# Kernel optimization log

Measured on AMD Instinct MI355X. Metric: run time of the kernel, lower is better.

The kernel has to match this reference:

```python
import jax, jax.numpy as jnp
import numpy as np

D = 128  # head dim

def setup_inputs() -> dict:
    key = jax.random.key(0)
    k1, k2, k3, k4, k5 = jax.random.split(key, 5)
    B, N, M, C1, C2 = 4, 4096, 4096, 1024, 1024
    x = jax.random.normal(k1, (B, N, C1), dtype=jnp.float32)
    y = jax.random.normal(k2, (B, M, C2), dtype=jnp.float32)
    # Linear(c, d, bias=False): out = inp @ W where W is [c, d]
    Wq = jax.random.normal(k3, (C1, D), dtype=jnp.float32) / np.sqrt(C1)
    Wk = jax.random.normal(k4, (C2, D), dtype=jnp.float32) / np.sqrt(C2)
    Wv = jax.random.normal(k5, (C2, D), dtype=jnp.float32) / np.sqrt(C2)
    return {"x": x, "y": y, "Wq": Wq, "Wk": Wk, "Wv": Wv}

def reference(x, y, Wq, Wk, Wv):
    q = x @ Wq                               # [B, N, d]
    k = y @ Wk                               # [B, M, d]
    v = y @ Wv                               # [B, M, d]
    scale = 1.0 / jnp.sqrt(jnp.asarray(D, dtype=q.dtype))
    a = jnp.einsum('bnd,bmd->bnm', q, k) * scale
    a = jax.nn.softmax(a, axis=-1)           # softmax FIRST
    a = jnp.triu(a, k=1)                     # post-softmax causal mask (keeps strict upper)
    out = jnp.einsum('bnm,bmd->bnd', a, v)   # [B, N, d]
    return out
```

## Files before the change

### kernel.cpp

```cpp
#include <hip/hip_runtime.h>
#include <hip/hip_bf16.h>
#include <stdint.h>


typedef __attribute__((ext_vector_type(8))) __bf16    bf16x8;
typedef __attribute__((ext_vector_type(4))) float     floatx4;
typedef __attribute__((ext_vector_type(8))) uint16_t  u16x8;
typedef __attribute__((ext_vector_type(4))) uint32_t  u32x4;

#define DEVFN __device__ __forceinline__

DEVFN uint16_t f32_to_bf16(float f) {
  uint32_t u = __builtin_bit_cast(uint32_t, f);
  u += 0x7FFFu + ((u >> 16) & 1u);
  return (uint16_t)(u >> 16);
}

DEVFN uint32_t bcast(float f) { return __builtin_bit_cast(uint32_t, f); }

DEVFN u32x4 pack_bf16_8(float4 a0, float4 a1) {
  uint32_t b0 = bcast(a0.x) + 0x8000u, b1 = bcast(a0.y) + 0x8000u;
  uint32_t b2 = bcast(a0.z) + 0x8000u, b3 = bcast(a0.w) + 0x8000u;
  uint32_t b4 = bcast(a1.x) + 0x8000u, b5 = bcast(a1.y) + 0x8000u;
  uint32_t b6 = bcast(a1.z) + 0x8000u, b7 = bcast(a1.w) + 0x8000u;
  u32x4 o;
  o[0] = (b0 >> 16) | (b1 & 0xFFFF0000u);
  o[1] = (b2 >> 16) | (b3 & 0xFFFF0000u);
  o[2] = (b4 >> 16) | (b5 & 0xFFFF0000u);
  o[3] = (b6 >> 16) | (b7 & 0xFFFF0000u);
  return o;
}

__global__ __launch_bounds__(256) void wt_kernel(
    const float* __restrict__ Wq, const float* __restrict__ Wk,
    const float* __restrict__ Wv, uint16_t* __restrict__ wt) {
  int tid = blockIdx.x * 256 + threadIdx.x;
  int mat = tid >> 14;
  int rem = tid & 16383;
  int n  = rem & 127;
  int k0 = rem >> 7;
  const float* W = (mat == 0) ? Wq : ((mat == 1) ? Wk : Wv);
  u16x8 v;
#pragma unroll
  for (int j = 0; j < 8; ++j) v[j] = f32_to_bf16(W[(k0 * 8 + j) * 128 + n]);
  *(u16x8*)&wt[mat * (128 * 1024) + n * 1024 + k0 * 8] = v;
}

__global__ __launch_bounds__(256) void qkv_kernel(
    const float* __restrict__ x, const float* __restrict__ y,
    const uint16_t* __restrict__ wt, uint16_t* __restrict__ q,
    uint16_t* __restrict__ k, uint16_t* __restrict__ vt) {
  constexpr int LDT = 72;
  constexpr int ABUF = 128 * LDT;
  __shared__ __align__(16) uint16_t sA[2 * ABUF];
  __shared__ __align__(16) uint16_t sW[2 * ABUF];
  const int t = threadIdx.x;
  const int mat = blockIdx.y, rt = blockIdx.x;
  const float* A = (mat == 0) ? x : y;
  const uint16_t* Wt = wt + mat * (128 * 1024);
  const int lane = t & 63, wv = t >> 6;
  const int cidx = lane & 15, quad = lane >> 4;
  const int sr = t >> 3;
  const int sc = (t & 7) * 8;
  const int Arow0 = rt * 128;

  floatx4 acc[2][8];
#pragma unroll
  for (int rg = 0; rg < 2; ++rg)
#pragma unroll
    for (int ng = 0; ng < 8; ++ng) acc[rg][ng] = (floatx4){0.f, 0.f, 0.f, 0.f};

  float4 a0r[4], a1r[4];
  u16x8 wr[4];
#pragma unroll
  for (int u = 0; u < 4; ++u) {
    int row = u * 32 + sr;
    const float* ap = &A[(size_t)(Arow0 + row) * 1024 + sc];
    a0r[u] = *(const float4*)ap;
    a1r[u] = *(const float4*)(ap + 4);
    wr[u]  = *(const u16x8*)&Wt[row * 1024 + sc];
  }
#pragma unroll
  for (int u = 0; u < 4; ++u) {
    int row = u * 32 + sr;
    *(u32x4*)&sA[row * LDT + sc] = pack_bf16_8(a0r[u], a1r[u]);
    *(u16x8*)&sW[row * LDT + sc] = wr[u];
  }
  __syncthreads();

  for (int kt = 0; kt < 16; ++kt) {
    const int cur = kt & 1, nxt = cur ^ 1;
    if (kt < 15) {
      const int kc = (kt + 1) * 64;
#pragma unroll
      for (int u = 0; u < 4; ++u) {
        int row = u * 32 + sr;
        const float* ap = &A[(size_t)(Arow0 + row) * 1024 + kc + sc];
        a0r[u] = *(const float4*)ap;
        a1r[u] = *(const float4*)(ap + 4);
        wr[u]  = *(const u16x8*)&Wt[row * 1024 + kc + sc];
      }
    }
    bf16x8 af[2][2];
#pragma unroll
    for (int rg = 0; rg < 2; ++rg)
#pragma unroll
      for (int ks = 0; ks < 2; ++ks)
        af[rg][ks] = *(const bf16x8*)
            &sA[cur * ABUF + (wv * 32 + rg * 16 + cidx) * LDT + ks * 32 + quad * 8];
#pragma unroll
    for (int ng = 0; ng < 8; ++ng) {
      bf16x8 b0 = *(const bf16x8*)&sW[cur * ABUF + (ng * 16 + cidx) * LDT + quad * 8];
      bf16x8 b1 = *(const bf16x8*)&sW[cur * ABUF + (ng * 16 + cidx) * LDT + 32 + quad * 8];
#pragma unroll
      for (int rg = 0; rg < 2; ++rg) {
        acc[rg][ng] = __builtin_amdgcn_mfma_f32_16x16x32_bf16(af[rg][0], b0, acc[rg][ng], 0, 0, 0);
        acc[rg][ng] = __builtin_amdgcn_mfma_f32_16x16x32_bf16(af[rg][1], b1, acc[rg][ng], 0, 0, 0);
      }
    }
    if (kt < 15) {
#pragma unroll
      for (int u = 0; u < 4; ++u) {
        int row = u * 32 + sr;
        *(u32x4*)&sA[nxt * ABUF + row * LDT + sc] = pack_bf16_8(a0r[u], a1r[u]);
        *(u16x8*)&sW[nxt * ABUF + row * LDT + sc] = wr[u];
      }
    }
    __syncthreads();
  }

  if (mat < 2) {
    uint16_t* outp = (mat == 0) ? q : k;
#pragma unroll
    for (int rg = 0; rg < 2; ++rg)
#pragma unroll
      for (int r = 0; r < 4; ++r) {
        int row = Arow0 + wv * 32 + rg * 16 + quad * 4 + r;
#pragma unroll
        for (int ng = 0; ng < 8; ++ng)
          outp[row * 128 + ng * 16 + cidx] = f32_to_bf16(acc[rg][ng][r]);
      }
  } else {
    int bq = rt >> 5;
    int mbase = (rt & 31) * 128;
#pragma unroll
    for (int rg = 0; rg < 2; ++rg)
#pragma unroll
      for (int r = 0; r < 4; ++r) {
        int m = mbase + wv * 32 + rg * 16 + quad * 4 + r;
#pragma unroll
        for (int ng = 0; ng < 8; ++ng)
          vt[(size_t)(bq * 128 + ng * 16 + cidx) * 4096 + m] = f32_to_bf16(acc[rg][ng][r]);
      }
  }
}

__global__ __launch_bounds__(256) void attn_kernel(
    const uint16_t* __restrict__ q, const uint16_t* __restrict__ k,
    const uint16_t* __restrict__ vt, float* __restrict__ opart,
    float* __restrict__ lpart) {
  constexpr int LDK = 136, LDV = 72, LDP = 72;
  constexpr int KBUF = 64 * LDK, VBUF = 128 * LDV;
  __shared__ __align__(16) uint16_t sK[2 * KBUF];
  __shared__ __align__(16) uint16_t sV[2 * VBUF];
  __shared__ __align__(16) uint16_t sP[4 * 16 * LDP];
  const int t = threadIdx.x;
  const int lane = t & 63, wv = t >> 6;
  const int cidx = lane & 15, quad = lane >> 4;
  const int qt = blockIdx.x, h = blockIdx.y, b = blockIdx.z;
  const int qmin = qt * 64 + wv * 16;
  const int mbase = h * 2048;

  const uint16_t* qb = q + (size_t)(b * 4096) * 128;
  const uint16_t* kb = k + (size_t)(b * 4096) * 128;
  const uint16_t* vb = vt + (size_t)(b * 128) * 4096;

  const float SC = 0.12751744610657223f;

  bf16x8 qf[4];
#pragma unroll
  for (int ks = 0; ks < 4; ++ks)
    qf[ks] = *(const bf16x8*)&qb[(qmin + cidx) * 128 + ks * 32 + quad * 8];

  floatx4 O[8];
#pragma unroll
  for (int dg = 0; dg < 8; ++dg) O[dg] = (floatx4){0.f, 0.f, 0.f, 0.f};
  float lst[4] = {0.f, 0.f, 0.f, 0.f};

  const int krow = t >> 4, kcol = (t & 15) * 8;
  const int vrow = t >> 3, vcol = (t & 7) * 8;

  u16x8 kr[4], vr[4];
#pragma unroll
  for (int u = 0; u < 4; ++u) {
    kr[u] = *(const u16x8*)&kb[(mbase + u * 16 + krow) * 128 + kcol];
    vr[u] = *(const u16x8*)&vb[(size_t)(u * 32 + vrow) * 4096 + mbase + vcol];
  }
#pragma unroll
  for (int u = 0; u < 4; ++u) {
    *(u16x8*)&sK[(u * 16 + krow) * LDK + kcol] = kr[u];
    *(u16x8*)&sV[(u * 32 + vrow) * LDV + vcol] = vr[u];
  }
  __syncthreads();

  for (int it = 0; it < 32; ++it) {
    const int m0 = mbase + it * 64;
    const int cur = it & 1, nxt = cur ^ 1;
    if (it < 31) {
      const int m1 = m0 + 64;
#pragma unroll
      for (int u = 0; u < 4; ++u) {
        kr[u] = *(const u16x8*)&kb[(m1 + u * 16 + krow) * 128 + kcol];
        vr[u] = *(const u16x8*)&vb[(size_t)(u * 32 + vrow) * 4096 + m1 + vcol];
      }
    }

    floatx4 accS[4];
#pragma unroll
    for (int ng = 0; ng < 4; ++ng) accS[ng] = (floatx4){0.f, 0.f, 0.f, 0.f};
#pragma unroll
    for (int ks = 0; ks < 4; ++ks)
#pragma unroll
      for (int ng = 0; ng < 4; ++ng) {
        bf16x8 bk = *(const bf16x8*)
            &sK[cur * KBUF + (ng * 16 + cidx) * LDK + ks * 32 + quad * 8];
        accS[ng] = __builtin_amdgcn_mfma_f32_16x16x32_bf16(qf[ks], bk, accS[ng], 0, 0, 0);
      }

    float p[4][4];
#pragma unroll
    for (int ng = 0; ng < 4; ++ng)
#pragma unroll
      for (int r = 0; r < 4; ++r) {
        p[ng][r] = exp2f(accS[ng][r] * SC);
        lst[r] += p[ng][r];
      }

    bool allmask = (m0 + 63) <= qmin;
    if (!allmask) {
      if (m0 <= qmin + 15) {
#pragma unroll
        for (int ng = 0; ng < 4; ++ng)
#pragma unroll
          for (int r = 0; r < 4; ++r) {
            int col = m0 + ng * 16 + cidx;
            int row = qmin + quad * 4 + r;
            if (col <= row) p[ng][r] = 0.f;
          }
      }
      uint16_t* pw = &sP[wv * 16 * LDP];
#pragma unroll
      for (int r = 0; r < 4; ++r)
#pragma unroll
        for (int ng = 0; ng < 4; ++ng) {
          uint32_t pb = bcast(p[ng][r]) + 0x8000u;
          pw[(quad * 4 + r) * LDP + ng * 16 + cidx] = (uint16_t)(pb >> 16);
        }
      asm volatile("s_waitcnt lgkmcnt(0)" ::: "memory");
      bf16x8 pa0 = *(const bf16x8*)&pw[cidx * LDP + quad * 8];
      bf16x8 pa1 = *(const bf16x8*)&pw[cidx * LDP + 32 + quad * 8];
#pragma unroll
      for (int dg = 0; dg < 8; ++dg) {
        bf16x8 v0 = *(const bf16x8*)&sV[cur * VBUF + (dg * 16 + cidx) * LDV + quad * 8];
        bf16x8 v1 = *(const bf16x8*)&sV[cur * VBUF + (dg * 16 + cidx) * LDV + 32 + quad * 8];
        O[dg] = __builtin_amdgcn_mfma_f32_16x16x32_bf16(pa0, v0, O[dg], 0, 0, 0);
        O[dg] = __builtin_amdgcn_mfma_f32_16x16x32_bf16(pa1, v1, O[dg], 0, 0, 0);
      }
    }

    if (it < 31) {
#pragma unroll
      for (int u = 0; u < 4; ++u) {
        *(u16x8*)&sK[nxt * KBUF + (u * 16 + krow) * LDK + kcol] = kr[u];
        *(u16x8*)&sV[nxt * VBUF + (u * 32 + vrow) * LDV + vcol] = vr[u];
      }
    }
    __syncthreads();
  }

#pragma unroll
  for (int r = 0; r < 4; ++r) {
#pragma unroll
    for (int s = 1; s < 16; s <<= 1) lst[r] += __shfl_xor(lst[r], s);
  }

  float* op = opart + (size_t)h * 2097152 + (size_t)b * 4096 * 128;
#pragma unroll
  for (int r = 0; r < 4; ++r) {
    int n = qmin + quad * 4 + r;
#pragma unroll
    for (int dg = 0; dg < 8; ++dg)
      op[(size_t)n * 128 + dg * 16 + cidx] = O[dg][r];
  }
  if (cidx == 0) {
#pragma unroll
    for (int r = 0; r < 4; ++r) {
      int n = qmin + quad * 4 + r;
      lpart[h * 16384 + b * 4096 + n] = lst[r];
    }
  }
}

__global__ __launch_bounds__(256) void combine_kernel(
    const float* __restrict__ opart, const float* __restrict__ lpart,
    float* __restrict__ out) {
  size_t i = (size_t)blockIdx.x * 256 + threadIdx.x;
  size_t e = i * 4;
  int row = (int)(e >> 7);
  float4 o0 = *(const float4*)&opart[e];
  float4 o1 = *(const float4*)&opart[2097152 + e];
  float inv = 1.0f / (lpart[row] + lpart[16384 + row]);
  float4 o;
  o.x = (o0.x + o1.x) * inv; o.y = (o0.y + o1.y) * inv;
  o.z = (o0.z + o1.z) * inv; o.w = (o0.w + o1.w) * inv;
  *(float4*)&out[e] = o;
}

extern "C" void kernel_launch(void* const* d_in, const int* in_sizes, int n_in,
                              void* d_out, int out_size, void* d_ws, size_t ws_size,
                              hipStream_t stream) {
  const float* x  = (const float*)d_in[0];
  const float* y  = (const float*)d_in[1];
  const float* Wq = (const float*)d_in[2];
  const float* Wk = (const float*)d_in[3];
  const float* Wv = (const float*)d_in[4];
  uint16_t* ws = (uint16_t*)d_ws;
  uint16_t* wt = ws;
  uint16_t* q  = ws + 393216;
  uint16_t* k  = q + 2097152;
  uint16_t* vt = k + 2097152;
  float* opart = (float*)((char*)d_ws + 13369344);
  float* lpart = opart + 4194304;
  float* o = (float*)d_out;

  hipLaunchKernelGGL(wt_kernel,      dim3(192),       dim3(256), 0, stream, Wq, Wk, Wv, wt);
  hipLaunchKernelGGL(qkv_kernel,     dim3(128, 3),    dim3(256), 0, stream, x, y, wt, q, k, vt);
  hipLaunchKernelGGL(attn_kernel,    dim3(64, 2, 4),  dim3(256), 0, stream, q, k, vt, opart, lpart);
  hipLaunchKernelGGL(combine_kernel, dim3(2048),      dim3(256), 0, stream, opart, lpart, o);
}
```

Measured before the change: 243.5 us.

## Split KV into more chunks, transpose MFMA, and shuffle P through registers

The attention kernel now computes S^T = K·Q^T so each lane owns one query row. P is passed into the PV MFMA with lane shuffles instead of a round trip through shared memory. K/V double buffering is dropped in favour of single-buffered LDS with a launch-bounds occupancy hint. When the workspace is large enough, the KV axis is split into 4 chunks instead of 2, giving more blocks, and the combine kernel sums a variable number of partials. The cost is lost prefetch overlap, which now relies on higher occupancy to hide latency, plus more partial-output traffic and combine work.

```diff
diff --git a/kernel.cpp b/kernel.cpp
--- a/kernel.cpp
+++ b/kernel.cpp
@@ -18,16 +18,16 @@
 
 DEVFN uint32_t bcast(float f) { return __builtin_bit_cast(uint32_t, f); }
 
+DEVFN uint32_t pack2_bf16(float a, float b) {
+  return ((bcast(a) + 0x8000u) >> 16) | ((bcast(b) + 0x8000u) & 0xFFFF0000u);
+}
+
 DEVFN u32x4 pack_bf16_8(float4 a0, float4 a1) {
-  uint32_t b0 = bcast(a0.x) + 0x8000u, b1 = bcast(a0.y) + 0x8000u;
-  uint32_t b2 = bcast(a0.z) + 0x8000u, b3 = bcast(a0.w) + 0x8000u;
-  uint32_t b4 = bcast(a1.x) + 0x8000u, b5 = bcast(a1.y) + 0x8000u;
-  uint32_t b6 = bcast(a1.z) + 0x8000u, b7 = bcast(a1.w) + 0x8000u;
   u32x4 o;
-  o[0] = (b0 >> 16) | (b1 & 0xFFFF0000u);
-  o[1] = (b2 >> 16) | (b3 & 0xFFFF0000u);
-  o[2] = (b4 >> 16) | (b5 & 0xFFFF0000u);
-  o[3] = (b6 >> 16) | (b7 & 0xFFFF0000u);
+  o[0] = pack2_bf16(a0.x, a0.y);
+  o[1] = pack2_bf16(a0.z, a0.w);
+  o[2] = pack2_bf16(a1.x, a1.y);
+  o[3] = pack2_bf16(a1.z, a1.w);
   return o;
 }
 
@@ -155,21 +155,19 @@
   }
 }
 
-__global__ __launch_bounds__(256) void attn_kernel(
+__global__ __launch_bounds__(256, 4) void attn_kernel(
     const uint16_t* __restrict__ q, const uint16_t* __restrict__ k,
     const uint16_t* __restrict__ vt, float* __restrict__ opart,
-    float* __restrict__ lpart) {
-  constexpr int LDK = 136, LDV = 72, LDP = 72;
-  constexpr int KBUF = 64 * LDK, VBUF = 128 * LDV;
-  __shared__ __align__(16) uint16_t sK[2 * KBUF];
-  __shared__ __align__(16) uint16_t sV[2 * VBUF];
-  __shared__ __align__(16) uint16_t sP[4 * 16 * LDP];
+    float* __restrict__ lpart, int mlen, int iters) {
+  constexpr int LDK = 136, LDV = 72;
+  __shared__ __align__(16) uint16_t sK[64 * LDK];
+  __shared__ __align__(16) uint16_t sV[128 * LDV];
   const int t = threadIdx.x;
   const int lane = t & 63, wv = t >> 6;
   const int cidx = lane & 15, quad = lane >> 4;
   const int qt = blockIdx.x, h = blockIdx.y, b = blockIdx.z;
   const int qmin = qt * 64 + wv * 16;
-  const int mbase = h * 2048;
+  const int mbase = h * mlen;
 
   const uint16_t* qb = q + (size_t)(b * 4096) * 128;
   const uint16_t* kb = k + (size_t)(b * 4096) * 128;
@@ -185,134 +183,116 @@
   floatx4 O[8];
 #pragma unroll
   for (int dg = 0; dg < 8; ++dg) O[dg] = (floatx4){0.f, 0.f, 0.f, 0.f};
-  float lst[4] = {0.f, 0.f, 0.f, 0.f};
+  float lsum = 0.f;
 
   const int krow = t >> 4, kcol = (t & 15) * 8;
   const int vrow = t >> 3, vcol = (t & 7) * 8;
 
-  u16x8 kr[4], vr[4];
-#pragma unroll
-  for (int u = 0; u < 4; ++u) {
-    kr[u] = *(const u16x8*)&kb[(mbase + u * 16 + krow) * 128 + kcol];
-    vr[u] = *(const u16x8*)&vb[(size_t)(u * 32 + vrow) * 4096 + mbase + vcol];
-  }
-#pragma unroll
-  for (int u = 0; u < 4; ++u) {
-    *(u16x8*)&sK[(u * 16 + krow) * LDK + kcol] = kr[u];
-    *(u16x8*)&sV[(u * 32 + vrow) * LDV + vcol] = vr[u];
-  }
-  __syncthreads();
-
-  for (int it = 0; it < 32; ++it) {
+  for (int it = 0; it < iters; ++it) {
     const int m0 = mbase + it * 64;
-    const int cur = it & 1, nxt = cur ^ 1;
-    if (it < 31) {
-      const int m1 = m0 + 64;
-#pragma unroll
-      for (int u = 0; u < 4; ++u) {
-        kr[u] = *(const u16x8*)&kb[(m1 + u * 16 + krow) * 128 + kcol];
-        vr[u] = *(const u16x8*)&vb[(size_t)(u * 32 + vrow) * 4096 + m1 + vcol];
-      }
-    }
-
-    floatx4 accS[4];
-#pragma unroll
-    for (int ng = 0; ng < 4; ++ng) accS[ng] = (floatx4){0.f, 0.f, 0.f, 0.f};
-#pragma unroll
-    for (int ks = 0; ks < 4; ++ks)
+    u16x8 kr[4], vr[4];
+#pragma unroll
+    for (int u = 0; u < 4; ++u) {
+      kr[u] = *(const u16x8*)&kb[(m0 + u * 16 + krow) * 128 + kcol];
+      vr[u] = *(const u16x8*)&vb[(size_t)(u * 32 + vrow) * 4096 + m0 + vcol];
+    }
+#pragma unroll
+    for (int u = 0; u < 4; ++u) {
+      *(u16x8*)&sK[(u * 16 + krow) * LDK + kcol] = kr[u];
+      *(u16x8*)&sV[(u * 32 + vrow) * LDV + vcol] = vr[u];
+    }
+    __syncthreads();
+
+    floatx4 accST[4];
+#pragma unroll
+    for (int ng = 0; ng < 4; ++ng) accST[ng] = (floatx4){0.f, 0.f, 0.f, 0.f};
+#pragma unroll
+    for (int ks = 0; ks < 4; ++ks) {
+      bf16x8 qv = qf[ks];
 #pragma unroll
       for (int ng = 0; ng < 4; ++ng) {
-        bf16x8 bk = *(const bf16x8*)
-            &sK[cur * KBUF + (ng * 16 + cidx) * LDK + ks * 32 + quad * 8];
-        accS[ng] = __builtin_amdgcn_mfma_f32_16x16x32_bf16(qf[ks], bk, accS[ng], 0, 0, 0);
-      }
+        bf16x8 kf = *(const bf16x8*)
+            &sK[(ng * 16 + cidx) * LDK + ks * 32 + quad * 8];
+        accST[ng] = __builtin_amdgcn_mfma_f32_16x16x32_bf16(kf, qv, accST[ng], 0, 0, 0);
+      }
+    }
 
     float p[4][4];
 #pragma unroll
     for (int ng = 0; ng < 4; ++ng)
 #pragma unroll
       for (int r = 0; r < 4; ++r) {
-        p[ng][r] = exp2f(accS[ng][r] * SC);
-        lst[r] += p[ng][r];
-      }
-
-    bool allmask = (m0 + 63) <= qmin;
-    if (!allmask) {
-      if (m0 <= qmin + 15) {
+        p[ng][r] = exp2f(accST[ng][r] * SC);
+        lsum += p[ng][r];
+      }
+
+    if (m0 + 63 > qmin) {
+      if (m0 < qmin + 16) {
 #pragma unroll
         for (int ng = 0; ng < 4; ++ng)
 #pragma unroll
           for (int r = 0; r < 4; ++r) {
-            int col = m0 + ng * 16 + cidx;
-            int row = qmin + quad * 4 + r;
-            if (col <= row) p[ng][r] = 0.f;
+            int m = m0 + ng * 16 + quad * 4 + r;
+            int n = qmin + cidx;
+            if (m <= n) p[ng][r] = 0.f;
           }
       }
-      uint16_t* pw = &sP[wv * 16 * LDP];
-#pragma unroll
-      for (int r = 0; r < 4; ++r)
-#pragma unroll
-        for (int ng = 0; ng < 4; ++ng) {
-          uint32_t pb = bcast(p[ng][r]) + 0x8000u;
-          pw[(quad * 4 + r) * LDP + ng * 16 + cidx] = (uint16_t)(pb >> 16);
+      uint32_t pk[4][2];
+#pragma unroll
+      for (int ng = 0; ng < 4; ++ng) {
+        pk[ng][0] = pack2_bf16(p[ng][0], p[ng][1]);
+        pk[ng][1] = pack2_bf16(p[ng][2], p[ng][3]);
+      }
+#pragma unroll
+      for (int ks = 0; ks < 2; ++ks) {
+        u32x4 pbw;
+#pragma unroll
+        for (int j2 = 0; j2 < 4; ++j2) {
+          int lr = ((quad & 1) << 3) + 2 * j2;
+          int srcl = ((lr >> 2) << 4) + cidx;
+          uint32_t lo = (uint32_t)__shfl((int)pk[2 * ks][j2 & 1], srcl);
+          uint32_t hi = (uint32_t)__shfl((int)pk[2 * ks + 1][j2 & 1], srcl);
+          pbw[j2] = (quad & 2) ? hi : lo;
         }
-      asm volatile("s_waitcnt lgkmcnt(0)" ::: "memory");
-      bf16x8 pa0 = *(const bf16x8*)&pw[cidx * LDP + quad * 8];
-      bf16x8 pa1 = *(const bf16x8*)&pw[cidx * LDP + 32 + quad * 8];
-#pragma unroll
-      for (int dg = 0; dg < 8; ++dg) {
-        bf16x8 v0 = *(const bf16x8*)&sV[cur * VBUF + (dg * 16 + cidx) * LDV + quad * 8];
-        bf16x8 v1 = *(const bf16x8*)&sV[cur * VBUF + (dg * 16 + cidx) * LDV + 32 + quad * 8];
-        O[dg] = __builtin_amdgcn_mfma_f32_16x16x32_bf16(pa0, v0, O[dg], 0, 0, 0);
-        O[dg] = __builtin_amdgcn_mfma_f32_16x16x32_bf16(pa1, v1, O[dg], 0, 0, 0);
-      }
-    }
-
-    if (it < 31) {
-#pragma unroll
-      for (int u = 0; u < 4; ++u) {
-        *(u16x8*)&sK[nxt * KBUF + (u * 16 + krow) * LDK + kcol] = kr[u];
-        *(u16x8*)&sV[nxt * VBUF + (u * 32 + vrow) * LDV + vcol] = vr[u];
+        bf16x8 pbv = __builtin_bit_cast(bf16x8, pbw);
+#pragma unroll
+        for (int dg = 0; dg < 8; ++dg) {
+          bf16x8 vf = *(const bf16x8*)
+              &sV[(dg * 16 + cidx) * LDV + ks * 32 + quad * 8];
+          O[dg] = __builtin_amdgcn_mfma_f32_16x16x32_bf16(vf, pbv, O[dg], 0, 0, 0);
+        }
       }
     }
     __syncthreads();
   }
 
-#pragma unroll
-  for (int r = 0; r < 4; ++r) {
-#pragma unroll
-    for (int s = 1; s < 16; s <<= 1) lst[r] += __shfl_xor(lst[r], s);
-  }
-
-  float* op = opart + (size_t)h * 2097152 + (size_t)b * 4096 * 128;
-#pragma unroll
-  for (int r = 0; r < 4; ++r) {
-    int n = qmin + quad * 4 + r;
-#pragma unroll
-    for (int dg = 0; dg < 8; ++dg)
-      op[(size_t)n * 128 + dg * 16 + cidx] = O[dg][r];
-  }
-  if (cidx == 0) {
-#pragma unroll
-    for (int r = 0; r < 4; ++r) {
-      int n = qmin + quad * 4 + r;
-      lpart[h * 16384 + b * 4096 + n] = lst[r];
-    }
-  }
+  lsum += __shfl_xor(lsum, 16);
+  lsum += __shfl_xor(lsum, 32);
+
+  const int n = qmin + cidx;
+  float* op = opart + ((size_t)h * 16384 + b * 4096 + n) * 128;
+#pragma unroll
+  for (int dg = 0; dg < 8; ++dg)
+    *(float4*)&op[dg * 16 + quad * 4] = __builtin_bit_cast(float4, O[dg]);
+  if (quad == 0) lpart[h * 16384 + b * 4096 + n] = lsum;
 }
 
 __global__ __launch_bounds__(256) void combine_kernel(
     const float* __restrict__ opart, const float* __restrict__ lpart,
-    float* __restrict__ out) {
+    float* __restrict__ out, int hcount) {
   size_t i = (size_t)blockIdx.x * 256 + threadIdx.x;
   size_t e = i * 4;
   int row = (int)(e >> 7);
-  float4 o0 = *(const float4*)&opart[e];
-  float4 o1 = *(const float4*)&opart[2097152 + e];
-  float inv = 1.0f / (lpart[row] + lpart[16384 + row]);
+  float4 acc = {0.f, 0.f, 0.f, 0.f};
+  float l = 0.f;
+  for (int h = 0; h < hcount; ++h) {
+    float4 ov = *(const float4*)&opart[(size_t)h * 2097152 + e];
+    acc.x += ov.x; acc.y += ov.y; acc.z += ov.z; acc.w += ov.w;
+    l += lpart[h * 16384 + row];
+  }
+  float inv = 1.0f / l;
   float4 o;
-  o.x = (o0.x + o1.x) * inv; o.y = (o0.y + o1.y) * inv;
-  o.z = (o0.z + o1.z) * inv; o.w = (o0.w + o1.w) * inv;
+  o.x = acc.x * inv; o.y = acc.y * inv; o.z = acc.z * inv; o.w = acc.w * inv;
   *(float4*)&out[e] = o;
 }
 
@@ -330,11 +310,13 @@
   uint16_t* k  = q + 2097152;
   uint16_t* vt = k + 2097152;
   float* opart = (float*)((char*)d_ws + 13369344);
-  float* lpart = opart + 4194304;
+  int hcount = (ws_size >= (size_t)13369344 + 4 * 8454144) ? 4 : 2;
+  float* lpart = opart + (size_t)hcount * 2097152;
   float* o = (float*)d_out;
-
-  hipLaunchKernelGGL(wt_kernel,      dim3(192),       dim3(256), 0, stream, Wq, Wk, Wv, wt);
-  hipLaunchKernelGGL(qkv_kernel,     dim3(128, 3),    dim3(256), 0, stream, x, y, wt, q, k, vt);
-  hipLaunchKernelGGL(attn_kernel,    dim3(64, 2, 4),  dim3(256), 0, stream, q, k, vt, opart, lpart);
-  hipLaunchKernelGGL(combine_kernel, dim3(2048),      dim3(256), 0, stream, opart, lpart, o);
-}
+  int mlen = 4096 / hcount, iters = mlen / 64;
+
+  hipLaunchKernelGGL(wt_kernel,      dim3(192),            dim3(256), 0, stream, Wq, Wk, Wv, wt);
+  hipLaunchKernelGGL(qkv_kernel,     dim3(128, 3),         dim3(256), 0, stream, x, y, wt, q, k, vt);
+  hipLaunchKernelGGL(attn_kernel,    dim3(64, hcount, 4),  dim3(256), 0, stream, q, k, vt, opart, lpart, mlen, iters);
+  hipLaunchKernelGGL(combine_kernel, dim3(2048),           dim3(256), 0, stream, opart, lpart, o, hcount);
+}
```

After: 240.7 us. About the same (-1.1%).
